# Performance work log

Hardware: AMD Instinct MI355X
Metric: run time of the kernel (lower is better)

Reference implementation:

```python
import jax, jax.numpy as jnp
import numpy as np

B, L, D = 4, 64, 512          # batch, trajectory length, d_model
DI, N, DC, R = 1024, 16, 4, 32  # d_inner, d_state, d_conv, dt_rank
NL = 4                         # n_layers
SD, AD, MEL = 17, 6, 1000      # state_dim, act_dim, max_ep_len
EPS = 1e-5


def setup_inputs() -> dict:
    key = jax.random.key(0)
    ks = iter(jax.random.split(key, 40))
    nrm = lambda shp, s=0.02: jax.random.normal(next(ks), shp, jnp.float32) * s
    inp = {
        "states": jax.random.normal(next(ks), (B, L, SD), jnp.float32),
        "actions": jax.random.normal(next(ks), (B, L, AD), jnp.float32),
        "returns_to_go": jax.random.normal(next(ks), (B, L, 1), jnp.float32),
        "constraints_to_go": jax.random.normal(next(ks), (B, L, 1), jnp.float32),
        "timesteps": jax.random.randint(next(ks), (B, L), 0, MEL, jnp.int32),
        # embedding / projection heads (torch Linear: y = x @ W.T + b)
        "es_w": nrm((D, SD)), "es_b": jnp.zeros((D,), jnp.float32),
        "ea_w": nrm((D, AD)), "ea_b": jnp.zeros((D,), jnp.float32),
        "er_w": nrm((D, 1)), "er_b": jnp.zeros((D,), jnp.float32),
        "ec_w": nrm((D, 1)), "ec_b": jnp.zeros((D,), jnp.float32),
        "et_w": nrm((MEL, D)),
        # per-layer Mamba params, stacked on leading NL axis
        "ln_w": jnp.ones((NL, D), jnp.float32), "ln_b": jnp.zeros((NL, D), jnp.float32),
        "in_w": nrm((NL, 2 * DI, D)),
        "conv_w": nrm((NL, DI, DC), 0.1), "conv_b": jnp.zeros((NL, DI), jnp.float32),
        "xp_w": nrm((NL, R + 2 * N, DI)),
        "dtp_w": nrm((NL, DI, R), 0.1),
        "dtp_b": jnp.full((NL, DI), -4.6, jnp.float32) + nrm((NL, DI), 0.1),
        "A_log": jnp.broadcast_to(jnp.log(jnp.arange(1, N + 1, dtype=jnp.float32)), (NL, DI, N)) * jnp.ones((NL, DI, 1), jnp.float32),
        "Dp": jnp.ones((NL, DI), jnp.float32),
        "out_w": nrm((NL, D, DI)),
        # final norm + heads
        "fn_w": jnp.ones((D,), jnp.float32), "fn_b": jnp.zeros((D,), jnp.float32),
        "ps_w": nrm((SD, D)), "ps_b": jnp.zeros((SD,), jnp.float32),
        "pa_w": nrm((AD, D)), "pa_b": jnp.zeros((AD,), jnp.float32),
    }
    return inp


def layernorm(x, w, b):
    mu = jnp.mean(x, -1, keepdims=True)
    var = jnp.mean(jnp.square(x - mu), -1, keepdims=True)
    return (x - mu) * jax.lax.rsqrt(var + EPS) * w + b


def selective_scan(u, delta, A, Bm, Cm, Dp):
    # u, delta: (B,T,DI); A: (DI,N); Bm, Cm: (B,T,N); Dp: (DI,)
    dA = jnp.exp(delta[..., None] * A)                      # (B,T,DI,N)
    dBu = delta[..., None] * Bm[:, :, None, :] * u[..., None]

    def step(h, xs):
        dA_t, dBu_t, C_t = xs
        h = dA_t * h + dBu_t                                # (B,DI,N)
        y = jnp.einsum('bdn,bn->bd', h, C_t)
        return h, y

    h0 = jnp.zeros((u.shape[0], u.shape[2], A.shape[1]), u.dtype)
    xs = (dA.transpose(1, 0, 2, 3), dBu.transpose(1, 0, 2, 3), Cm.transpose(1, 0, 2))
    _, ys = jax.lax.scan(step, h0, xs)
    return ys.transpose(1, 0, 2) + u * Dp


def mamba_mixer(x, in_w, conv_w, conv_b, xp_w, dtp_w, dtp_b, A_log, Dp, out_w):
    T = x.shape[1]
    xz = x @ in_w.T                                         # (B,T,2*DI)
    xm, z = jnp.split(xz, 2, axis=-1)
    # causal depthwise conv1d, kernel DC
    xpad = jnp.pad(xm, ((0, 0), (DC - 1, 0), (0, 0)))
    xc = sum(xpad[:, k:k + T, :] * conv_w[:, k] for k in range(DC)) + conv_b
    xc = jax.nn.silu(xc)
    dbc = xc @ xp_w.T                                       # (B,T,R+2N)
    dt, Bm, Cm = jnp.split(dbc, [R, R + N], axis=-1)
    delta = jax.nn.softplus(dt @ dtp_w.T + dtp_b)           # (B,T,DI)
    y = selective_scan(xc, delta, -jnp.exp(A_log), Bm, Cm, Dp)
    y = y * jax.nn.silu(z)
    return y @ out_w.T


def reference(states, actions, returns_to_go, constraints_to_go, timesteps,
              es_w, es_b, ea_w, ea_b, er_w, er_b, ec_w, ec_b, et_w,
              ln_w, ln_b, in_w, conv_w, conv_b, xp_w, dtp_w, dtp_b, A_log, Dp, out_w,
              fn_w, fn_b, ps_w, ps_b, pa_w, pa_b):
    te = et_w[timesteps]                                    # (B,L,D)
    se = states @ es_w.T + es_b + te
    ae = actions @ ea_w.T + ea_b + te
    re = returns_to_go @ er_w.T + er_b + te
    ce = constraints_to_go @ ec_w.T + ec_b + te
    # interleave (r, c, s, a) per timestep -> (B, 4L, D)
    x = jnp.stack((re, ce, se, ae), axis=2).reshape(B, 4 * L, D)
    for i in range(NL):
        x = x + mamba_mixer(layernorm(x, ln_w[i], ln_b[i]),
                            in_w[i], conv_w[i], conv_b[i], xp_w[i],
                            dtp_w[i], dtp_b[i], A_log[i], Dp[i], out_w[i])
    x = layernorm(x, fn_w, fn_b)
    outputs = x.reshape(B, L, 4, D).transpose(0, 2, 1, 3)   # (B,4,L,D)
    state_preds = outputs[:, 3] @ ps_w.T + ps_b             # from action tokens
    action_preds = outputs[:, 2] @ pa_w.T + pa_b            # from state tokens
    return state_preds, action_preds
```

## Files before the change

### kernel.cpp

```cpp
#include <hip/hip_runtime.h>
#include <math.h>

#define B_ 4
#define L_ 64
#define D_ 512
#define DI_ 1024
#define N_ 16
#define DC_ 4
#define R_ 32
#define NL_ 4
#define SD_ 17
#define AD_ 6
#define T_ 256
#define CH3_ 32
#define TC3_ 8
#define DL3_ 8

#define NW_IN  (NL_ * 2 * DI_ * D_)
#define NW_OUT (NL_ * D_ * DI_)
#define NW_XP  (NL_ * 64 * DI_)
#define NW_TOT (NW_IN + NW_OUT + NW_XP)

typedef short bf16x8 __attribute__((ext_vector_type(8)));
typedef float f32x4 __attribute__((ext_vector_type(4)));

__device__ __forceinline__ float silu_f(float v) { return v / (1.f + __expf(-v)); }
__device__ __forceinline__ float softplus_f(float v) {
    return fmaxf(v, 0.f) + log1pf(__expf(-fabsf(v)));
}
__device__ __forceinline__ unsigned short f2bs(float f) {
    unsigned u = __float_as_uint(f);
    u += 0x7fffu + ((u >> 16) & 1u);
    return (unsigned short)(u >> 16);
}
__device__ __forceinline__ float bs2f(unsigned short s) {
    return __uint_as_float(((unsigned)s) << 16);
}

__global__ __launch_bounds__(256) void wcvt_kernel(
    const float* __restrict__ in_w, const float* __restrict__ out_w,
    const float* __restrict__ xp_w, unsigned short* __restrict__ wb)
{
    const int i = blockIdx.x * 256 + threadIdx.x;
    if (i >= NW_TOT / 4) return;
    const int e = i * 4;
    const float* src; int off;
    if (e < NW_IN)               { src = in_w;  off = e; }
    else if (e < NW_IN + NW_OUT) { src = out_w; off = e - NW_IN; }
    else                         { src = xp_w;  off = e - NW_IN - NW_OUT; }
    const float4 v = *(const float4*)(src + off);
    ushort4 o;
    o.x = f2bs(v.x); o.y = f2bs(v.y); o.z = f2bs(v.z); o.w = f2bs(v.w);
    *(ushort4*)(wb + e) = o;
}

__global__ __launch_bounds__(512) void embed_kernel(
    const float* __restrict__ states, const float* __restrict__ actions,
    const float* __restrict__ rtg, const float* __restrict__ ctg,
    const int* __restrict__ ts,
    const float* __restrict__ es_w, const float* __restrict__ es_b,
    const float* __restrict__ ea_w, const float* __restrict__ ea_b,
    const float* __restrict__ er_w, const float* __restrict__ er_b,
    const float* __restrict__ ec_w, const float* __restrict__ ec_b,
    const float* __restrict__ et_w, float* __restrict__ x)
{
    const int bl = blockIdx.x;
    const int d = threadIdx.x;
    const float te = et_w[(size_t)ts[bl] * D_ + d];
    const float r = rtg[bl] * er_w[d] + er_b[d] + te;
    const float c = ctg[bl] * ec_w[d] + ec_b[d] + te;
    float s = es_b[d] + te;
#pragma unroll
    for (int k = 0; k < SD_; ++k) s += states[bl * SD_ + k] * es_w[d * SD_ + k];
    float a = ea_b[d] + te;
#pragma unroll
    for (int k = 0; k < AD_; ++k) a += actions[bl * AD_ + k] * ea_w[d * AD_ + k];
    float* xp = x + (size_t)bl * 4 * D_;
    xp[0 * D_ + d] = r;
    xp[1 * D_ + d] = c;
    xp[2 * D_ + d] = s;
    xp[3 * D_ + d] = a;
}

template <int MODE>
__global__ __launch_bounds__(256) void ln2_kernel(
    float* __restrict__ x, const float* __restrict__ p0,
    const float* __restrict__ p1,
    const float* __restrict__ w, const float* __restrict__ b,
    void* __restrict__ o_)
{
    const int tok = blockIdx.x;
    const int tid = threadIdx.x;
    float2 v = reinterpret_cast<float2*>(x + (size_t)tok * D_)[tid];
    if (MODE >= 1) {
        const float2 a0 = reinterpret_cast<const float2*>(p0 + (size_t)tok * D_)[tid];
        const float2 a1 = reinterpret_cast<const float2*>(p1 + (size_t)tok * D_)[tid];
        v.x += a0.x + a1.x;
        v.y += a0.y + a1.y;
        reinterpret_cast<float2*>(x + (size_t)tok * D_)[tid] = v;
    }
    float s = v.x + v.y;
#pragma unroll
    for (int off = 1; off < 64; off <<= 1) s += __shfl_xor(s, off);
    __shared__ float red[8];
    const int wv = tid >> 6;
    if ((tid & 63) == 0) red[wv] = s;
    __syncthreads();
    const float mean = (red[0] + red[1] + red[2] + red[3]) * (1.f / D_);
    const float dx = v.x - mean, dy = v.y - mean;
    float q = dx * dx + dy * dy;
#pragma unroll
    for (int off = 1; off < 64; off <<= 1) q += __shfl_xor(q, off);
    if ((tid & 63) == 0) red[4 + wv] = q;
    __syncthreads();
    const float var = (red[4] + red[5] + red[6] + red[7]) * (1.f / D_);
    const float r = rsqrtf(var + 1e-5f);
    const int d0 = tid * 2;
    const float o0 = dx * r * w[d0] + b[d0];
    const float o1 = dy * r * w[d0 + 1] + b[d0 + 1];
    if (MODE == 2) {
        float* o = (float*)o_;
        o[(size_t)tok * D_ + d0] = o0;
        o[(size_t)tok * D_ + d0 + 1] = o1;
    } else {
        unsigned short* o = (unsigned short*)o_;
        o[(size_t)tok * D_ + d0] = f2bs(o0);
        o[(size_t)tok * D_ + d0 + 1] = f2bs(o1);
    }
}

template <int MR, int NR, int EPI, int KT>
__global__ __launch_bounds__(256) void gemm3(
    const unsigned short* __restrict__ A, int lda,
    const unsigned short* __restrict__ W, int ldw,
    float* __restrict__ C, unsigned short* __restrict__ Cb1,
    unsigned short* __restrict__ Cb2, int N)
{
    const int lane = threadIdx.x & 63, wid = threadIdx.x >> 6;
    const int r = lane & 15, kq = lane >> 4;
    const int wm = blockIdx.y * (2 * MR * 16) + (wid >> 1) * (MR * 16);
    const int wn = blockIdx.x * (2 * NR * 16) + (wid & 1) * (NR * 16);
    const int kb = (EPI == 4) ? blockIdx.z * KT : 0;
    f32x4 acc[MR][NR] = {};
#pragma unroll 4
    for (int k0 = 0; k0 < KT; k0 += 32) {
        bf16x8 a[MR], b[NR];
#pragma unroll
        for (int i = 0; i < MR; ++i)
            a[i] = *(const bf16x8*)(A + (size_t)(wm + i * 16 + r) * lda + kb + k0 + kq * 8);
#pragma unroll
        for (int j = 0; j < NR; ++j)
            b[j] = *(const bf16x8*)(W + (size_t)(wn + j * 16 + r) * ldw + kb + k0 + kq * 8);
#pragma unroll
        for (int i = 0; i < MR; ++i)
#pragma unroll
            for (int j = 0; j < NR; ++j)
                acc[i][j] = __builtin_amdgcn_mfma_f32_16x16x32_bf16(a[i], b[j], acc[i][j], 0, 0, 0);
    }
#pragma unroll
    for (int i = 0; i < MR; ++i)
#pragma unroll
        for (int j = 0; j < NR; ++j)
#pragma unroll
            for (int g = 0; g < 4; ++g) {
                const int row = wm + i * 16 + kq * 4 + g;
                const int col = wn + j * 16 + r;
                const float val = acc[i][j][g];
                if (EPI == 3) {
                    if (col < DI_) Cb1[(size_t)row * DI_ + col] = f2bs(val);
                    else Cb2[(size_t)row * DI_ + (col - DI_)] = f2bs(silu_f(val));
                } else if (EPI == 4) {
                    C[(size_t)blockIdx.z * (1024 * 512) + (size_t)row * 512 + col] = val;
                } else {
                    C[(size_t)row * N + col] = val;
                }
            }
}

__global__ __launch_bounds__(256) void conv_kernel(
    const unsigned short* __restrict__ xmb, const float* __restrict__ cw,
    const float* __restrict__ cb, unsigned short* __restrict__ xcb)
{
    const int e0 = (blockIdx.x * 256 + threadIdx.x) * 8;
    const int d0 = e0 & (DI_ - 1);
    const int bt = e0 >> 10;
    const int t = bt & (T_ - 1);
    float4 w4[8];
#pragma unroll
    for (int j = 0; j < 8; ++j) w4[j] = ((const float4*)cw)[d0 + j];
    float acc[8];
#pragma unroll
    for (int j = 0; j < 8; ++j) acc[j] = cb[d0 + j];
#pragma unroll
    for (int k = 0; k < DC_; ++k) {
        if (t - 3 + k >= 0) {
            const bf16x8 v = *(const bf16x8*)(xmb + (size_t)(bt - 3 + k) * DI_ + d0);
#pragma unroll
            for (int j = 0; j < 8; ++j) {
                const float wk = (k == 0) ? w4[j].x : (k == 1) ? w4[j].y
                               : (k == 2) ? w4[j].z : w4[j].w;
                acc[j] += wk * bs2f((unsigned short)v[j]);
            }
        }
    }
    bf16x8 ov;
#pragma unroll
    for (int j = 0; j < 8; ++j) ov[j] = (short)f2bs(silu_f(acc[j]));
    *(bf16x8*)(xcb + e0) = ov;
}

__global__ __launch_bounds__(256) void xp_kernel(
    const unsigned short* __restrict__ xcb, const unsigned short* __restrict__ Wb,
    float* __restrict__ dbc)
{
    __shared__ float red[4][16][64];
    const int tid = threadIdx.x;
    const int wid = tid >> 6, lane = tid & 63;
    const int r = lane & 15, kq = lane >> 4;
    const int m0 = blockIdx.x * 16;
    f32x4 acc4[4] = {};
    const int k00 = wid * 256;
#pragma unroll
    for (int ks = 0; ks < 8; ++ks) {
        const int k0 = k00 + ks * 32;
        const bf16x8 a = *(const bf16x8*)(xcb + (size_t)(m0 + r) * DI_ + k0 + kq * 8);
#pragma unroll
        for (int j = 0; j < 4; ++j) {
            const bf16x8 bfr = *(const bf16x8*)(Wb + (size_t)(j * 16 + r) * DI_ + k0 + kq * 8);
            acc4[j] = __builtin_amdgcn_mfma_f32_16x16x32_bf16(a, bfr, acc4[j], 0, 0, 0);
        }
    }
#pragma unroll
    for (int j = 0; j < 4; ++j)
#pragma unroll
        for (int g = 0; g < 4; ++g)
            red[wid][kq * 4 + g][j * 16 + r] = acc4[j][g];
    __syncthreads();
    for (int i = tid; i < 1024; i += 256) {
        const int row = i >> 6, col = i & 63;
        const float s = red[0][row][col] + red[1][row][col] +
                        red[2][row][col] + red[3][row][col];
        dbc[(size_t)(m0 + row) * 64 + col] = s;
    }
}

__global__ __launch_bounds__(256, 3) void scan_kernel(
    const unsigned short* __restrict__ xcb, const float* __restrict__ dbc,
    const float* __restrict__ dtw, const float* __restrict__ dtbias,
    const float* __restrict__ A_log, const float* __restrict__ Dp,
    const unsigned short* __restrict__ zs, unsigned short* __restrict__ ygb)
{
    __shared__ float dlt_s[T_][DL3_ + 1];
    __shared__ float Sl[CH3_][DL3_][17];
    __shared__ float Pl[CH3_][DL3_][17];
    const int tid = threadIdx.x;
    const int dl = tid & (DL3_ - 1);
    const int c = tid >> 3;
    const int b = blockIdx.x >> 7;
    const int d = (blockIdx.x & 127) * DL3_ + dl;
    const int row0 = b * T_ + c * TC3_;
    {
        const float4* Wp = (const float4*)(dtw + (size_t)d * R_);
        float4 w4[8];
#pragma unroll
        for (int q = 0; q < 8; ++q) w4[q] = Wp[q];
        const float bias = dtbias[d];
#pragma unroll
        for (int t = 0; t < TC3_; ++t) {
            const float4* Ap = (const float4*)(dbc + (size_t)(row0 + t) * 64);
            float acc = bias;
#pragma unroll
            for (int q = 0; q < 8; ++q) {
                const float4 a4 = Ap[q];
                acc += a4.x * w4[q].x + a4.y * w4[q].y + a4.z * w4[q].z + a4.w * w4[q].w;
            }
            dlt_s[c * TC3_ + t][dl] = softplus_f(acc);
        }
    }
    float Av[N_];
    {
        const float4* Alp = (const float4*)(A_log + (size_t)d * N_);
#pragma unroll
        for (int q = 0; q < 4; ++q) {
            const float4 v = Alp[q];
            Av[q * 4 + 0] = -__expf(v.x);
            Av[q * 4 + 1] = -__expf(v.y);
            Av[q * 4 + 2] = -__expf(v.z);
            Av[q * 4 + 3] = -__expf(v.w);
        }
    }
    __syncthreads();
    const unsigned short* up = xcb + (size_t)row0 * DI_ + d;
    const float* bc = dbc + (size_t)row0 * 64;
    float h[N_];
#pragma unroll
    for (int n = 0; n < N_; ++n) h[n] = 0.f;
    float dsum = 0.f;
#pragma unroll
    for (int t = 0; t < TC3_; ++t) {
        const float dt_t = dlt_s[c * TC3_ + t][dl];
        dsum += dt_t;
        const float dbu = dt_t * bs2f(up[t * DI_]);
#pragma unroll
        for (int q = 0; q < 4; ++q) {
            const float4 b4 = *(const float4*)(bc + t * 64 + R_ + q * 4);
            h[q * 4 + 0] = __expf(dt_t * Av[q * 4 + 0]) * h[q * 4 + 0] + dbu * b4.x;
            h[q * 4 + 1] = __expf(dt_t * Av[q * 4 + 1]) * h[q * 4 + 1] + dbu * b4.y;
            h[q * 4 + 2] = __expf(dt_t * Av[q * 4 + 2]) * h[q * 4 + 2] + dbu * b4.z;
            h[q * 4 + 3] = __expf(dt_t * Av[q * 4 + 3]) * h[q * 4 + 3] + dbu * b4.w;
        }
    }
#pragma unroll
    for (int n = 0; n < N_; ++n) {
        Sl[c][dl][n] = h[n];
        Pl[c][dl][n] = __expf(Av[n] * dsum);
    }
    __syncthreads();
    if (tid < DL3_ * N_) {
        const int dd = tid >> 4, nn = tid & 15;
        float hin = 0.f;
#pragma unroll
        for (int c2 = 0; c2 < CH3_; ++c2) {
            const float t2 = Pl[c2][dd][nn] * hin + Sl[c2][dd][nn];
            Sl[c2][dd][nn] = hin;
            hin = t2;
        }
    }
    __syncthreads();
#pragma unroll
    for (int n = 0; n < N_; ++n) h[n] = Sl[c][dl][n];
    const float Dd = Dp[d];
    const unsigned short* zp = zs + (size_t)row0 * DI_ + d;
    unsigned short* yp = ygb + (size_t)row0 * DI_ + d;
#pragma unroll
    for (int t = 0; t < TC3_; ++t) {
        const float dt_t = dlt_s[c * TC3_ + t][dl];
        const float ut = bs2f(up[t * DI_]);
        const float dbu = dt_t * ut;
        float y = ut * Dd;
#pragma unroll
        for (int q = 0; q < 4; ++q) {
            const float4 b4 = *(const float4*)(bc + t * 64 + R_ + q * 4);
            const float4 c4 = *(const float4*)(bc + t * 64 + R_ + N_ + q * 4);
            h[q * 4 + 0] = __expf(dt_t * Av[q * 4 + 0]) * h[q * 4 + 0] + dbu * b4.x;
            h[q * 4 + 1] = __expf(dt_t * Av[q * 4 + 1]) * h[q * 4 + 1] + dbu * b4.y;
            h[q * 4 + 2] = __expf(dt_t * Av[q * 4 + 2]) * h[q * 4 + 2] + dbu * b4.z;
            h[q * 4 + 3] = __expf(dt_t * Av[q * 4 + 3]) * h[q * 4 + 3] + dbu * b4.w;
            y += h[q * 4 + 0] * c4.x + h[q * 4 + 1] * c4.y
               + h[q * 4 + 2] * c4.z + h[q * 4 + 3] * c4.w;
        }
        yp[t * DI_] = f2bs(y * bs2f(zp[t * DI_]));
    }
}

__global__ __launch_bounds__(256) void heads_kernel(
    const float* __restrict__ xn,
    const float* __restrict__ ps_w, const float* __restrict__ ps_b,
    const float* __restrict__ pa_w, const float* __restrict__ pa_b,
    float* __restrict__ out)
{
    const int idx = blockIdx.x * 4 + (threadIdx.x >> 6);
    const int lane = threadIdx.x & 63;
    const int bl = idx / 23, j = idx % 23;
    const float* tok;
    const float* wrow;
    float bias;
    float* dst;
    if (j < SD_) {
        tok = xn + ((size_t)bl * 4 + 3) * D_;
        wrow = ps_w + (size_t)j * D_;
        bias = ps_b[j];
        dst = out + (size_t)bl * SD_ + j;
    } else {
        const int jj = j - SD_;
        tok = xn + ((size_t)bl * 4 + 2) * D_;
        wrow = pa_w + (size_t)jj * D_;
        bias = pa_b[jj];
        dst = out + (size_t)B_ * L_ * SD_ + (size_t)bl * AD_ + jj;
    }
    float s = 0.f;
    for (int dd = lane; dd < D_; dd += 64) s += tok[dd] * wrow[dd];
#pragma unroll
    for (int off = 1; off < 64; off <<= 1) s += __shfl_xor(s, off);
    if (lane == 0) *dst = s + bias;
}

extern "C" void kernel_launch(void* const* d_in, const int* in_sizes, int n_in,
                              void* d_out, int out_size, void* d_ws, size_t ws_size,
                              hipStream_t stream)
{
    const float* states  = (const float*)d_in[0];
    const float* actions = (const float*)d_in[1];
    const float* rtg     = (const float*)d_in[2];
    const float* ctg     = (const float*)d_in[3];
    const int*   ts      = (const int*)d_in[4];
    const float* es_w = (const float*)d_in[5];  const float* es_b = (const float*)d_in[6];
    const float* ea_w = (const float*)d_in[7];  const float* ea_b = (const float*)d_in[8];
    const float* er_w = (const float*)d_in[9];  const float* er_b = (const float*)d_in[10];
    const float* ec_w = (const float*)d_in[11]; const float* ec_b = (const float*)d_in[12];
    const float* et_w = (const float*)d_in[13];
    const float* ln_w = (const float*)d_in[14]; const float* ln_b = (const float*)d_in[15];
    const float* in_w = (const float*)d_in[16];
    const float* conv_w = (const float*)d_in[17]; const float* conv_b = (const float*)d_in[18];
    const float* xp_w = (const float*)d_in[19];
    const float* dtp_w = (const float*)d_in[20]; const float* dtp_b = (const float*)d_in[21];
    const float* A_log = (const float*)d_in[22]; const float* Dp = (const float*)d_in[23];
    const float* out_w = (const float*)d_in[24];
    const float* fn_w = (const float*)d_in[25]; const float* fn_b = (const float*)d_in[26];
    const float* ps_w = (const float*)d_in[27]; const float* ps_b = (const float*)d_in[28];
    const float* pa_w = (const float*)d_in[29]; const float* pa_b = (const float*)d_in[30];
    float* out = (float*)d_out;

    float* ws   = (float*)d_ws;
    float* x    = ws;
    float* xn   = x + 524288;
    float* p    = xn + 524288;
    float* dbc  = p + 1048576;
    unsigned short* xnb = (unsigned short*)(dbc + 65536);
    unsigned short* xmb = xnb + 524288;
    unsigned short* xcb = xmb + 1048576;
    unsigned short* zs  = xcb + 1048576;
    unsigned short* ygb = zs + 1048576;
    unsigned short* wb  = ygb + 1048576;
    unsigned short* wb_in  = wb;
    unsigned short* wb_out = wb + NW_IN;
    unsigned short* wb_xp  = wb + NW_IN + NW_OUT;

    wcvt_kernel<<<(NW_TOT / 4 + 255) / 256, 256, 0, stream>>>(in_w, out_w, xp_w, wb);
    embed_kernel<<<B_ * L_, D_, 0, stream>>>(states, actions, rtg, ctg, ts,
        es_w, es_b, ea_w, ea_b, er_w, er_b, ec_w, ec_b, et_w, x);

    for (int i = 0; i < NL_; ++i) {
        if (i == 0)
            ln2_kernel<0><<<B_ * T_, 256, 0, stream>>>(
                x, nullptr, nullptr, ln_w, ln_b, xnb);
        else
            ln2_kernel<1><<<B_ * T_, 256, 0, stream>>>(
                x, p, p + 524288, ln_w + i * D_, ln_b + i * D_, xnb);
        gemm3<2, 2, 3, 512><<<dim3(32, 16), 256, 0, stream>>>(
            xnb, D_, wb_in + (size_t)i * 2 * DI_ * D_, D_, nullptr, xmb, zs, 2 * DI_);
        conv_kernel<<<512, 256, 0, stream>>>(
            xmb, conv_w + i * DI_ * DC_, conv_b + i * DI_, xcb);
        xp_kernel<<<64, 256, 0, stream>>>(
            xcb, wb_xp + (size_t)i * 64 * DI_, dbc);
        scan_kernel<<<B_ * (DI_ / DL3_), 256, 0, stream>>>(
            xcb, dbc, dtp_w + (size_t)i * DI_ * R_, dtp_b + i * DI_,
            A_log + (size_t)i * DI_ * N_, Dp + i * DI_, zs, ygb);
        gemm3<2, 2, 4, 512><<<dim3(8, 16, 2), 256, 0, stream>>>(
            ygb, DI_, wb_out + (size_t)i * D_ * DI_, DI_, p, nullptr, nullptr, D_);
    }

    ln2_kernel<2><<<B_ * T_, 256, 0, stream>>>(x, p, p + 524288, fn_w, fn_b, xn);
    heads_kernel<<<(B_ * L_ * 23) / 4, 256, 0, stream>>>(xn, ps_w, ps_b, pa_w, pa_b, out);
}
```

Baseline: 289.2 us.

## Fuse conv into in-projection, residual add into out-projection, merge init kernels

The causal depthwise conv is folded into the in-projection GEMM epilogue. Each x-part tile also computes a 16-row halo, stages the result in shared memory and applies conv and SiLU, so the separate conv kernel and the xm round trip go away. The out-projection becomes a single-K, 16-row-tile GEMM that adds straight into the residual x, which removes the split-K partial buffers and the residual add in layernorm. Weight conversion and embedding are merged into one launch. The cost is redundant halo MFMA work, and the out-projection now uses smaller tiles with less reuse.

```diff
diff --git a/kernel.cpp b/kernel.cpp
--- a/kernel.cpp
+++ b/kernel.cpp
@@ -20,6 +20,7 @@
 #define NW_OUT (NL_ * D_ * DI_)
 #define NW_XP  (NL_ * 64 * DI_)
 #define NW_TOT (NW_IN + NW_OUT + NW_XP)
+#define WCVT_BLOCKS (NW_TOT / 4 / 256)
 
 typedef short bf16x8 __attribute__((ext_vector_type(8)));
 typedef float f32x4 __attribute__((ext_vector_type(4)));
@@ -37,24 +38,9 @@
     return __uint_as_float(((unsigned)s) << 16);
 }
 
-__global__ __launch_bounds__(256) void wcvt_kernel(
+__global__ __launch_bounds__(256) void init_kernel(
     const float* __restrict__ in_w, const float* __restrict__ out_w,
-    const float* __restrict__ xp_w, unsigned short* __restrict__ wb)
-{
-    const int i = blockIdx.x * 256 + threadIdx.x;
-    if (i >= NW_TOT / 4) return;
-    const int e = i * 4;
-    const float* src; int off;
-    if (e < NW_IN)               { src = in_w;  off = e; }
-    else if (e < NW_IN + NW_OUT) { src = out_w; off = e - NW_IN; }
-    else                         { src = xp_w;  off = e - NW_IN - NW_OUT; }
-    const float4 v = *(const float4*)(src + off);
-    ushort4 o;
-    o.x = f2bs(v.x); o.y = f2bs(v.y); o.z = f2bs(v.z); o.w = f2bs(v.w);
-    *(ushort4*)(wb + e) = o;
-}
-
-__global__ __launch_bounds__(512) void embed_kernel(
+    const float* __restrict__ xp_w, unsigned short* __restrict__ wb,
     const float* __restrict__ states, const float* __restrict__ actions,
     const float* __restrict__ rtg, const float* __restrict__ ctg,
     const int* __restrict__ ts,
@@ -64,41 +50,48 @@
     const float* __restrict__ ec_w, const float* __restrict__ ec_b,
     const float* __restrict__ et_w, float* __restrict__ x)
 {
-    const int bl = blockIdx.x;
-    const int d = threadIdx.x;
-    const float te = et_w[(size_t)ts[bl] * D_ + d];
-    const float r = rtg[bl] * er_w[d] + er_b[d] + te;
-    const float c = ctg[bl] * ec_w[d] + ec_b[d] + te;
-    float s = es_b[d] + te;
-#pragma unroll
-    for (int k = 0; k < SD_; ++k) s += states[bl * SD_ + k] * es_w[d * SD_ + k];
-    float a = ea_b[d] + te;
-#pragma unroll
-    for (int k = 0; k < AD_; ++k) a += actions[bl * AD_ + k] * ea_w[d * AD_ + k];
-    float* xp = x + (size_t)bl * 4 * D_;
-    xp[0 * D_ + d] = r;
-    xp[1 * D_ + d] = c;
-    xp[2 * D_ + d] = s;
-    xp[3 * D_ + d] = a;
-}
-
-template <int MODE>
-__global__ __launch_bounds__(256) void ln2_kernel(
-    float* __restrict__ x, const float* __restrict__ p0,
-    const float* __restrict__ p1,
-    const float* __restrict__ w, const float* __restrict__ b,
-    void* __restrict__ o_)
+    if (blockIdx.x < WCVT_BLOCKS) {
+        const int i = blockIdx.x * 256 + threadIdx.x;
+        const int e = i * 4;
+        const float* src; int off;
+        if (e < NW_IN)               { src = in_w;  off = e; }
+        else if (e < NW_IN + NW_OUT) { src = out_w; off = e - NW_IN; }
+        else                         { src = xp_w;  off = e - NW_IN - NW_OUT; }
+        const float4 v = *(const float4*)(src + off);
+        ushort4 o;
+        o.x = f2bs(v.x); o.y = f2bs(v.y); o.z = f2bs(v.z); o.w = f2bs(v.w);
+        *(ushort4*)(wb + e) = o;
+    } else {
+        const int bl = blockIdx.x - WCVT_BLOCKS;
+#pragma unroll
+        for (int j = 0; j < 2; ++j) {
+            const int d = threadIdx.x + j * 256;
+            const float te = et_w[(size_t)ts[bl] * D_ + d];
+            const float r = rtg[bl] * er_w[d] + er_b[d] + te;
+            const float c = ctg[bl] * ec_w[d] + ec_b[d] + te;
+            float s = es_b[d] + te;
+#pragma unroll
+            for (int k = 0; k < SD_; ++k) s += states[bl * SD_ + k] * es_w[d * SD_ + k];
+            float a = ea_b[d] + te;
+#pragma unroll
+            for (int k = 0; k < AD_; ++k) a += actions[bl * AD_ + k] * ea_w[d * AD_ + k];
+            float* xp = x + (size_t)bl * 4 * D_;
+            xp[0 * D_ + d] = r;
+            xp[1 * D_ + d] = c;
+            xp[2 * D_ + d] = s;
+            xp[3 * D_ + d] = a;
+        }
+    }
+}
+
+template <bool BF16OUT>
+__global__ __launch_bounds__(256) void ln_kernel(
+    const float* __restrict__ x, const float* __restrict__ w,
+    const float* __restrict__ b, void* __restrict__ o_)
 {
     const int tok = blockIdx.x;
     const int tid = threadIdx.x;
-    float2 v = reinterpret_cast<float2*>(x + (size_t)tok * D_)[tid];
-    if (MODE >= 1) {
-        const float2 a0 = reinterpret_cast<const float2*>(p0 + (size_t)tok * D_)[tid];
-        const float2 a1 = reinterpret_cast<const float2*>(p1 + (size_t)tok * D_)[tid];
-        v.x += a0.x + a1.x;
-        v.y += a0.y + a1.y;
-        reinterpret_cast<float2*>(x + (size_t)tok * D_)[tid] = v;
-    }
+    const float2 v = reinterpret_cast<const float2*>(x + (size_t)tok * D_)[tid];
     float s = v.x + v.y;
 #pragma unroll
     for (int off = 1; off < 64; off <<= 1) s += __shfl_xor(s, off);
@@ -118,95 +111,104 @@
     const int d0 = tid * 2;
     const float o0 = dx * r * w[d0] + b[d0];
     const float o1 = dy * r * w[d0 + 1] + b[d0 + 1];
-    if (MODE == 2) {
+    if (BF16OUT) {
+        unsigned short* o = (unsigned short*)o_;
+        o[(size_t)tok * D_ + d0] = f2bs(o0);
+        o[(size_t)tok * D_ + d0 + 1] = f2bs(o1);
+    } else {
         float* o = (float*)o_;
         o[(size_t)tok * D_ + d0] = o0;
         o[(size_t)tok * D_ + d0 + 1] = o1;
-    } else {
-        unsigned short* o = (unsigned short*)o_;
-        o[(size_t)tok * D_ + d0] = f2bs(o0);
-        o[(size_t)tok * D_ + d0 + 1] = f2bs(o1);
-    }
-}
-
-template <int MR, int NR, int EPI, int KT>
-__global__ __launch_bounds__(256) void gemm3(
-    const unsigned short* __restrict__ A, int lda,
-    const unsigned short* __restrict__ W, int ldw,
-    float* __restrict__ C, unsigned short* __restrict__ Cb1,
-    unsigned short* __restrict__ Cb2, int N)
-{
+    }
+}
+
+__global__ __launch_bounds__(256) void inproj_kernel(
+    const unsigned short* __restrict__ A, const unsigned short* __restrict__ W,
+    const float* __restrict__ cw, const float* __restrict__ cb,
+    unsigned short* __restrict__ xcb, unsigned short* __restrict__ zs)
+{
+    __shared__ unsigned short sxm[80][72];
     const int lane = threadIdx.x & 63, wid = threadIdx.x >> 6;
     const int r = lane & 15, kq = lane >> 4;
-    const int wm = blockIdx.y * (2 * MR * 16) + (wid >> 1) * (MR * 16);
-    const int wn = blockIdx.x * (2 * NR * 16) + (wid & 1) * (NR * 16);
-    const int kb = (EPI == 4) ? blockIdx.z * KT : 0;
-    f32x4 acc[MR][NR] = {};
+    const int m0 = blockIdx.y * 64;
+    const int n0 = blockIdx.x * 64;
+    const bool is_xm = (n0 < DI_);
+    const int wm = m0 + (wid >> 1) * 32;
+    const int wn = n0 + (wid & 1) * 32;
+    f32x4 acc[2][2] = {};
+    f32x4 accx[2] = {};
+    int xrow = m0 - 16 + r;
+    if (xrow < 0) xrow = 0;
 #pragma unroll 4
-    for (int k0 = 0; k0 < KT; k0 += 32) {
-        bf16x8 a[MR], b[NR];
-#pragma unroll
-        for (int i = 0; i < MR; ++i)
-            a[i] = *(const bf16x8*)(A + (size_t)(wm + i * 16 + r) * lda + kb + k0 + kq * 8);
-#pragma unroll
-        for (int j = 0; j < NR; ++j)
-            b[j] = *(const bf16x8*)(W + (size_t)(wn + j * 16 + r) * ldw + kb + k0 + kq * 8);
-#pragma unroll
-        for (int i = 0; i < MR; ++i)
-#pragma unroll
-            for (int j = 0; j < NR; ++j)
+    for (int k0 = 0; k0 < D_; k0 += 32) {
+        bf16x8 a[2], b[2];
+#pragma unroll
+        for (int i = 0; i < 2; ++i)
+            a[i] = *(const bf16x8*)(A + (size_t)(wm + i * 16 + r) * D_ + k0 + kq * 8);
+#pragma unroll
+        for (int j = 0; j < 2; ++j)
+            b[j] = *(const bf16x8*)(W + (size_t)(wn + j * 16 + r) * D_ + k0 + kq * 8);
+#pragma unroll
+        for (int i = 0; i < 2; ++i)
+#pragma unroll
+            for (int j = 0; j < 2; ++j)
                 acc[i][j] = __builtin_amdgcn_mfma_f32_16x16x32_bf16(a[i], b[j], acc[i][j], 0, 0, 0);
-    }
-#pragma unroll
-    for (int i = 0; i < MR; ++i)
-#pragma unroll
-        for (int j = 0; j < NR; ++j)
+        if (is_xm) {
+            const bf16x8 ax = *(const bf16x8*)(A + (size_t)xrow * D_ + k0 + kq * 8);
+#pragma unroll
+            for (int j = 0; j < 2; ++j)
+                accx[j] = __builtin_amdgcn_mfma_f32_16x16x32_bf16(ax, b[j], accx[j], 0, 0, 0);
+        }
+    }
+    if (!is_xm) {
+#pragma unroll
+        for (int i = 0; i < 2; ++i)
+#pragma unroll
+            for (int j = 0; j < 2; ++j)
+#pragma unroll
+                for (int g = 0; g < 4; ++g) {
+                    const int row = wm + i * 16 + kq * 4 + g;
+                    const int col = wn + j * 16 + r - DI_;
+                    zs[(size_t)row * DI_ + col] = f2bs(silu_f(acc[i][j][g]));
+                }
+        return;
+    }
+#pragma unroll
+    for (int i = 0; i < 2; ++i)
+#pragma unroll
+        for (int j = 0; j < 2; ++j)
 #pragma unroll
             for (int g = 0; g < 4; ++g) {
-                const int row = wm + i * 16 + kq * 4 + g;
-                const int col = wn + j * 16 + r;
-                const float val = acc[i][j][g];
-                if (EPI == 3) {
-                    if (col < DI_) Cb1[(size_t)row * DI_ + col] = f2bs(val);
-                    else Cb2[(size_t)row * DI_ + (col - DI_)] = f2bs(silu_f(val));
-                } else if (EPI == 4) {
-                    C[(size_t)blockIdx.z * (1024 * 512) + (size_t)row * 512 + col] = val;
-                } else {
-                    C[(size_t)row * N + col] = val;
-                }
+                const int srow = 16 + (wm - m0) + i * 16 + kq * 4 + g;
+                const int scol = (wn - n0) + j * 16 + r;
+                sxm[srow][scol] = f2bs(acc[i][j][g]);
             }
-}
-
-__global__ __launch_bounds__(256) void conv_kernel(
-    const unsigned short* __restrict__ xmb, const float* __restrict__ cw,
-    const float* __restrict__ cb, unsigned short* __restrict__ xcb)
-{
-    const int e0 = (blockIdx.x * 256 + threadIdx.x) * 8;
-    const int d0 = e0 & (DI_ - 1);
-    const int bt = e0 >> 10;
-    const int t = bt & (T_ - 1);
-    float4 w4[8];
-#pragma unroll
-    for (int j = 0; j < 8; ++j) w4[j] = ((const float4*)cw)[d0 + j];
-    float acc[8];
-#pragma unroll
-    for (int j = 0; j < 8; ++j) acc[j] = cb[d0 + j];
-#pragma unroll
-    for (int k = 0; k < DC_; ++k) {
-        if (t - 3 + k >= 0) {
-            const bf16x8 v = *(const bf16x8*)(xmb + (size_t)(bt - 3 + k) * DI_ + d0);
-#pragma unroll
-            for (int j = 0; j < 8; ++j) {
-                const float wk = (k == 0) ? w4[j].x : (k == 1) ? w4[j].y
-                               : (k == 2) ? w4[j].z : w4[j].w;
-                acc[j] += wk * bs2f((unsigned short)v[j]);
+#pragma unroll
+    for (int j = 0; j < 2; ++j)
+#pragma unroll
+        for (int g = 0; g < 4; ++g) {
+            const int srow = kq * 4 + g;
+            const int scol = (wn - n0) + j * 16 + r;
+            sxm[srow][scol] = f2bs(accx[j][g]);
+        }
+    __syncthreads();
+    for (int e = threadIdx.x; e < 64 * 64; e += 256) {
+        const int col = e & 63, rrel = e >> 6;
+        const int grow = m0 + rrel;
+        const int t = grow & (T_ - 1);
+        const int d = n0 + col;
+        const float4 w4 = ((const float4*)cw)[d];
+        float a = cb[d];
+#pragma unroll
+        for (int k = 0; k < DC_; ++k) {
+            if (t - 3 + k >= 0) {
+                const float wk = (k == 0) ? w4.x : (k == 1) ? w4.y
+                               : (k == 2) ? w4.z : w4.w;
+                a += wk * bs2f(sxm[16 + rrel - 3 + k][col]);
             }
         }
-    }
-    bf16x8 ov;
-#pragma unroll
-    for (int j = 0; j < 8; ++j) ov[j] = (short)f2bs(silu_f(acc[j]));
-    *(bf16x8*)(xcb + e0) = ov;
+        xcb[(size_t)grow * DI_ + d] = f2bs(silu_f(a));
+    }
 }
 
 __global__ __launch_bounds__(256) void xp_kernel(
@@ -350,6 +352,29 @@
                + h[q * 4 + 2] * c4.z + h[q * 4 + 3] * c4.w;
         }
         yp[t * DI_] = f2bs(y * bs2f(zp[t * DI_]));
+    }
+}
+
+__global__ __launch_bounds__(256) void outproj_kernel(
+    const unsigned short* __restrict__ A, const unsigned short* __restrict__ W,
+    float* __restrict__ x)
+{
+    const int lane = threadIdx.x & 63, w = threadIdx.x >> 6;
+    const int r = lane & 15, kq = lane >> 4;
+    const int m0 = blockIdx.y * 16;
+    const int wn = blockIdx.x * 64 + w * 16;
+    f32x4 acc = {};
+#pragma unroll 4
+    for (int k0 = 0; k0 < DI_; k0 += 32) {
+        const bf16x8 a = *(const bf16x8*)(A + (size_t)(m0 + r) * DI_ + k0 + kq * 8);
+        const bf16x8 b = *(const bf16x8*)(W + (size_t)(wn + r) * DI_ + k0 + kq * 8);
+        acc = __builtin_amdgcn_mfma_f32_16x16x32_bf16(a, b, acc, 0, 0, 0);
+    }
+#pragma unroll
+    for (int g = 0; g < 4; ++g) {
+        const int row = m0 + kq * 4 + g;
+        const int col = wn + r;
+        x[(size_t)row * D_ + col] += acc[g];
     }
 }
 
@@ -414,11 +439,9 @@
     float* ws   = (float*)d_ws;
     float* x    = ws;
     float* xn   = x + 524288;
-    float* p    = xn + 524288;
-    float* dbc  = p + 1048576;
+    float* dbc  = xn + 524288;
     unsigned short* xnb = (unsigned short*)(dbc + 65536);
-    unsigned short* xmb = xnb + 524288;
-    unsigned short* xcb = xmb + 1048576;
+    unsigned short* xcb = xnb + 524288;
     unsigned short* zs  = xcb + 1048576;
     unsigned short* ygb = zs + 1048576;
     unsigned short* wb  = ygb + 1048576;
@@ -426,30 +449,26 @@
     unsigned short* wb_out = wb + NW_IN;
     unsigned short* wb_xp  = wb + NW_IN + NW_OUT;
 
-    wcvt_kernel<<<(NW_TOT / 4 + 255) / 256, 256, 0, stream>>>(in_w, out_w, xp_w, wb);
-    embed_kernel<<<B_ * L_, D_, 0, stream>>>(states, actions, rtg, ctg, ts,
+    init_kernel<<<WCVT_BLOCKS + B_ * L_, 256, 0, stream>>>(
+        in_w, out_w, xp_w, wb,
+        states, actions, rtg, ctg, ts,
         es_w, es_b, ea_w, ea_b, er_w, er_b, ec_w, ec_b, et_w, x);
 
     for (int i = 0; i < NL_; ++i) {
-        if (i == 0)
-            ln2_kernel<0><<<B_ * T_, 256, 0, stream>>>(
-                x, nullptr, nullptr, ln_w, ln_b, xnb);
-        else
-            ln2_kernel<1><<<B_ * T_, 256, 0, stream>>>(
-                x, p, p + 524288, ln_w + i * D_, ln_b + i * D_, xnb);
-        gemm3<2, 2, 3, 512><<<dim3(32, 16), 256, 0, stream>>>(
-            xnb, D_, wb_in + (size_t)i * 2 * DI_ * D_, D_, nullptr, xmb, zs, 2 * DI_);
-        conv_kernel<<<512, 256, 0, stream>>>(
-            xmb, conv_w + i * DI_ * DC_, conv_b + i * DI_, xcb);
+        ln_kernel<true><<<B_ * T_, 256, 0, stream>>>(
+            x, ln_w + i * D_, ln_b + i * D_, xnb);
+        inproj_kernel<<<dim3(32, 16), 256, 0, stream>>>(
+            xnb, wb_in + (size_t)i * 2 * DI_ * D_,
+            conv_w + i * DI_ * DC_, conv_b + i * DI_, xcb, zs);
         xp_kernel<<<64, 256, 0, stream>>>(
             xcb, wb_xp + (size_t)i * 64 * DI_, dbc);
         scan_kernel<<<B_ * (DI_ / DL3_), 256, 0, stream>>>(
             xcb, dbc, dtp_w + (size_t)i * DI_ * R_, dtp_b + i * DI_,
             A_log + (size_t)i * DI_ * N_, Dp + i * DI_, zs, ygb);
-        gemm3<2, 2, 4, 512><<<dim3(8, 16, 2), 256, 0, stream>>>(
-            ygb, DI_, wb_out + (size_t)i * D_ * DI_, DI_, p, nullptr, nullptr, D_);
-    }
-
-    ln2_kernel<2><<<B_ * T_, 256, 0, stream>>>(x, p, p + 524288, fn_w, fn_b, xn);
+        outproj_kernel<<<dim3(8, 64), 256, 0, stream>>>(
+            ygb, wb_out + (size_t)i * D_ * DI_, x);
+    }
+
+    ln_kernel<false><<<B_ * T_, 256, 0, stream>>>(x, fn_w, fn_b, xn);
     heads_kernel<<<(B_ * L_ * 23) / 4, 256, 0, stream>>>(xn, ps_w, ps_b, pa_w, pa_b, out);
 }
```

After: 310.4 us. 7.3% more time.
